# Kernel tuning notes

Hardware: AMD Instinct MI355X
Metric: run time of the kernel (lower is better)

Reference implementation:

```python
import jax, jax.numpy as jnp
import numpy as np

N, E, G = 10000, 160000, 64
NODE_DIM, HID = 128, 256


def _edge_conv(x, src, dst, w1, b1, w2, b2):
    # gather endpoints: x_i = target features, x_j = source features (PyG source_to_target)
    x_i = x[dst]                              # [E, C]
    x_j = x[src]                              # [E, C]
    m = jnp.concatenate([x_i, x_j - x_i], axis=-1)  # [E, 2C]
    m = jax.nn.relu(m @ w1 + b1) @ w2 + b2          # [E, H]
    out = jax.ops.segment_max(m, dst, num_segments=N)  # scatter-max per target node
    return out  # nodes with no in-edges get -inf; subsequent relu maps them to 0 (matches PyG fill 0 + relu)


def setup_inputs() -> dict:
    key = jax.random.key(0)
    ks = jax.random.split(key, 20)
    x = jax.random.normal(ks[0], (N, NODE_DIM), dtype=jnp.float32)
    edge_index = jax.random.randint(ks[1], (2, E), 0, N)
    batch = jnp.sort(jax.random.randint(ks[2], (N,), 0, G))
    s = 0.05
    inp = {"x": x, "edge_index": edge_index, "batch": batch}
    dims = [(2 * NODE_DIM, HID), (2 * HID, HID), (2 * HID, HID)]
    for li, (din, dout) in enumerate(dims):
        inp[f"c{li}_w1"] = jax.random.normal(ks[3 + 4 * li], (din, dout), jnp.float32) * s
        inp[f"c{li}_b1"] = jnp.zeros((dout,), jnp.float32)
        inp[f"c{li}_w2"] = jax.random.normal(ks[4 + 4 * li], (dout, dout), jnp.float32) * s
        inp[f"c{li}_b2"] = jnp.zeros((dout,), jnp.float32)
    inp["cl_w1"] = jax.random.normal(ks[15], (2 * HID, HID), jnp.float32) * s
    inp["cl_b1"] = jnp.zeros((HID,), jnp.float32)
    inp["cl_w2"] = jax.random.normal(ks[16], (HID, 64), jnp.float32) * s
    inp["cl_b2"] = jnp.zeros((64,), jnp.float32)
    inp["cl_w3"] = jax.random.normal(ks[17], (64, 1), jnp.float32) * s
    inp["cl_b3"] = jnp.zeros((1,), jnp.float32)
    return inp


def reference(x, edge_index, batch,
              c0_w1, c0_b1, c0_w2, c0_b2,
              c1_w1, c1_b1, c1_w2, c1_b2,
              c2_w1, c2_b1, c2_w2, c2_b2,
              cl_w1, cl_b1, cl_w2, cl_b2, cl_w3, cl_b3):
    src, dst = edge_index[0], edge_index[1]
    for (w1, b1, w2, b2) in [(c0_w1, c0_b1, c0_w2, c0_b2),
                             (c1_w1, c1_b1, c1_w2, c1_b2),
                             (c2_w1, c2_b1, c2_w2, c2_b2)]:
        x = jax.nn.relu(_edge_conv(x, src, dst, w1, b1, w2, b2))
    # global mean / max pool per graph
    sums = jax.ops.segment_sum(x, batch, num_segments=G)
    counts = jax.ops.segment_sum(jnp.ones((x.shape[0], 1), x.dtype), batch, num_segments=G)
    x_mean = sums / jnp.maximum(counts, 1.0)
    x_max = jax.ops.segment_max(x, batch, num_segments=G)
    x_max = jnp.where(counts > 0, x_max, 0.0)
    h = jnp.concatenate([x_mean, x_max], axis=1)  # [G, 2H]
    h = jax.nn.relu(h @ cl_w1 + cl_b1)            # dropout is eval-mode identity
    h = jax.nn.relu(h @ cl_w2 + cl_b2)
    out = (h @ cl_w3 + cl_b3).squeeze(-1)         # [G]
    return out
```

## Files before the change

kernel.cpp:

```cpp
#include <hip/hip_runtime.h>


#define NN 10000
#define NE 160000
#define NG 64
#define NP 10048
#define EB 64

typedef __attribute__((ext_vector_type(8))) _Float16 f16x8;
typedef __attribute__((ext_vector_type(4))) _Float16 f16x4;
typedef __attribute__((ext_vector_type(4))) float f32x4;

__global__ void hist_kernel(const int* __restrict__ dstI, int* __restrict__ hist) {
    int i = blockIdx.x * blockDim.x + threadIdx.x;
    if (i < NE) atomicAdd(&hist[dstI[i]], 1);
}

__global__ void scan_kernel(const int* __restrict__ hist, int* __restrict__ cursor) {
    __shared__ int sums[256];
    const int t = threadIdx.x;
    const int per = (NN + 255) / 256;
    const int lo = t * per, hi = (lo + per < NN) ? lo + per : NN;
    int s = 0;
    for (int i = lo; i < hi; ++i) s += hist[i];
    sums[t] = s;
    __syncthreads();
    for (int ofs = 1; ofs < 256; ofs <<= 1) {
        int add = (t >= ofs) ? sums[t - ofs] : 0;
        __syncthreads();
        sums[t] += add;
        __syncthreads();
    }
    int run = sums[t] - s;
    for (int i = lo; i < hi; ++i) {
        int h = hist[i];
        cursor[i] = run;
        run += h;
    }
}

__global__ void scatter_kernel(const int* __restrict__ srcI, const int* __restrict__ dstI,
                               int* __restrict__ cursor,
                               int* __restrict__ se2, int* __restrict__ de2) {
    int i = blockIdx.x * blockDim.x + threadIdx.x;
    if (i < NE) {
        int d = dstI[i];
        int p = atomicAdd(&cursor[d], 1);
        se2[p] = srcI[i];
        de2[p] = d;
    }
}

__global__ void prep_weights(const float* __restrict__ w1, const float* __restrict__ w2, int C,
                             _Float16* __restrict__ WcT, _Float16* __restrict__ w2T) {
    int total1 = 512 * C;
    int total = total1 + 256 * 256;
    for (int i = blockIdx.x * blockDim.x + threadIdx.x; i < total; i += gridDim.x * blockDim.x) {
        if (i < total1) {
            int n = i / C, k = i - n * C;
            float v = (n < 256) ? (w1[k * 256 + n] - w1[(C + k) * 256 + n])
                                : w1[(C + k) * 256 + (n - 256)];
            WcT[n * C + k] = (_Float16)v;
        } else {
            int j = i - total1;
            int n = j >> 8, k = j & 255;
            w2T[n * 256 + k] = (_Float16)w2[k * 256 + n];
        }
    }
}

__global__ void conv_rows(const float* __restrict__ src, int C, _Float16* __restrict__ xh) {
    int total = NP * C;
    for (int i = blockIdx.x * blockDim.x + threadIdx.x; i < total; i += gridDim.x * blockDim.x) {
        int row = i / C;
        xh[i] = (_Float16)((row < NN) ? src[i] : 0.f);
    }
}

template <int C>
__global__ __launch_bounds__(256) void node_gemm(
    const _Float16* __restrict__ xh, const _Float16* __restrict__ WT,
    const float* __restrict__ b1, float* __restrict__ AB) {
    const int wave = threadIdx.x >> 6, lane = threadIdx.x & 63;
    const int lrow = lane & 15, lk = (lane >> 4) * 8;
    const int r0 = blockIdx.x * 64;
    const int c0 = blockIdx.y * 128 + wave * 32;

    f32x4 acc[4][2] = {};
#pragma unroll
    for (int kk = 0; kk < C; kk += 32) {
        f16x8 ah[4];
#pragma unroll
        for (int m = 0; m < 4; ++m)
            ah[m] = *(const f16x8*)(xh + (size_t)(r0 + m * 16 + lrow) * C + kk + lk);
#pragma unroll
        for (int t = 0; t < 2; ++t) {
            f16x8 bh = *(const f16x8*)(WT + (size_t)(c0 + t * 16 + lrow) * C + kk + lk);
#pragma unroll
            for (int m = 0; m < 4; ++m)
                acc[m][t] = __builtin_amdgcn_mfma_f32_16x16x32_f16(ah[m], bh, acc[m][t], 0, 0, 0);
        }
    }
#pragma unroll
    for (int t = 0; t < 2; ++t) {
        const int col = c0 + t * 16 + lrow;
        const float bias = (col < 256) ? b1[col] : 0.f;
#pragma unroll
        for (int m = 0; m < 4; ++m) {
#pragma unroll
            for (int j = 0; j < 4; ++j) {
                const int row = r0 + m * 16 + (lane >> 4) * 4 + j;
                AB[(size_t)row * 512 + col] = acc[m][t][j] + bias;
            }
        }
    }
}

__global__ __launch_bounds__(256, 3) void edge_gemm(
    const float* __restrict__ AB,
    const int* __restrict__ se2, const int* __restrict__ de2,
    const _Float16* __restrict__ w2T,
    const float* __restrict__ b2, float* __restrict__ y) {
    __shared__ _Float16 hh[EB * 256];
    const int tid = threadIdx.x;
    const int wave = tid >> 6, lane = tid & 63;
    const int e0 = blockIdx.x * EB;
    const int ew = wave * 16;

    int se[16], de[16];
#pragma unroll
    for (int i = 0; i < 16; ++i) {
        se[i] = se2[e0 + ew + i];
        de[i] = de2[e0 + ew + i];
    }
#pragma unroll
    for (int b = 0; b < 4; ++b) {
        float4 av[4], bv[4];
#pragma unroll
        for (int i = 0; i < 4; ++i) {
            const int el = b * 4 + i;
            av[i] = *(const float4*)(AB + (size_t)de[el] * 512 + lane * 4);
            bv[i] = *(const float4*)(AB + (size_t)se[el] * 512 + 256 + lane * 4);
        }
#pragma unroll
        for (int i = 0; i < 4; ++i) {
            const int row = b * 16 + wave * 4 + i;
            f16x4 vh;
            vh[0] = (_Float16)fmaxf(av[i].x + bv[i].x, 0.f);
            vh[1] = (_Float16)fmaxf(av[i].y + bv[i].y, 0.f);
            vh[2] = (_Float16)fmaxf(av[i].z + bv[i].z, 0.f);
            vh[3] = (_Float16)fmaxf(av[i].w + bv[i].w, 0.f);
            const int idx = (row * 256 + lane * 4) ^ ((row & 7) << 3);
            *(f16x4*)(&hh[idx]) = vh;
        }
    }
    __syncthreads();

    const int lrow = lane & 15, lk = (lane >> 4) * 8;
    const _Float16* wbase = w2T + (size_t)(wave * 64 + lrow) * 256 + lk;

    f16x8 bhA[4], bhB[4];
#pragma unroll
    for (int t = 0; t < 4; ++t)
        bhA[t] = *(const f16x8*)(wbase + (size_t)(t * 16) * 256);

    f32x4 acc[4][4] = {};
#pragma unroll
    for (int kk = 0; kk < 256; kk += 32) {
        if (kk + 32 < 256) {
#pragma unroll
            for (int t = 0; t < 4; ++t)
                bhB[t] = *(const f16x8*)(wbase + (size_t)(t * 16) * 256 + kk + 32);
        }
        f16x8 ah[4];
#pragma unroll
        for (int m = 0; m < 4; ++m) {
            const int row = m * 16 + lrow;
            const int idx = (row * 256 + kk + lk) ^ ((row & 7) << 3);
            ah[m] = *(const f16x8*)(&hh[idx]);
        }
#pragma unroll
        for (int t = 0; t < 4; ++t)
#pragma unroll
            for (int m = 0; m < 4; ++m)
                acc[m][t] = __builtin_amdgcn_mfma_f32_16x16x32_f16(ah[m], bhA[t], acc[m][t], 0, 0, 0);
#pragma unroll
        for (int t = 0; t < 4; ++t) bhA[t] = bhB[t];
    }

    const int g = lane >> 4;
    int d[16];
#pragma unroll
    for (int k = 0; k < 16; ++k) d[k] = de2[e0 + g * 16 + k];
#pragma unroll
    for (int t = 0; t < 4; ++t) {
        const int col = wave * 64 + t * 16 + lrow;
        const float bias = b2[col];
        float run = acc[0][t][0] + bias;
        int dp = d[0];
#pragma unroll
        for (int k = 1; k < 16; ++k) {
            const float v = acc[k >> 2][t][k & 3] + bias;
            if (d[k] == dp) {
                run = fmaxf(run, v);
            } else {
                if (run > 0.f) atomicMax((int*)(y + (size_t)dp * 256 + col), __float_as_int(run));
                run = v;
                dp = d[k];
            }
        }
        if (run > 0.f) atomicMax((int*)(y + (size_t)dp * 256 + col), __float_as_int(run));
    }
}

__global__ void pool_kernel(const float* __restrict__ y, const int* __restrict__ batch,
                            float* __restrict__ pooled) {
    const int g = blockIdx.x;
    __shared__ int slo, shi;
    if (threadIdx.x == 0) {
        int lo = 0, hi = NN;
        while (lo < hi) { int m = (lo + hi) >> 1; if (batch[m] < g) lo = m + 1; else hi = m; }
        slo = lo;
        int lo2 = lo, hi2 = NN;
        while (lo2 < hi2) { int m = (lo2 + hi2) >> 1; if (batch[m] < g + 1) lo2 = m + 1; else hi2 = m; }
        shi = lo2;
    }
    __syncthreads();
    const int lo = slo, hi = shi, c = threadIdx.x;
    float s0 = 0.f, s1 = 0.f, s2 = 0.f, s3 = 0.f;
    float m0 = 0.f, m1 = 0.f, m2 = 0.f, m3 = 0.f;
    int n = lo;
    for (; n + 4 <= hi; n += 4) {
        float v0 = y[(size_t)(n + 0) * 256 + c];
        float v1 = y[(size_t)(n + 1) * 256 + c];
        float v2 = y[(size_t)(n + 2) * 256 + c];
        float v3 = y[(size_t)(n + 3) * 256 + c];
        s0 += v0; s1 += v1; s2 += v2; s3 += v3;
        m0 = fmaxf(m0, v0); m1 = fmaxf(m1, v1); m2 = fmaxf(m2, v2); m3 = fmaxf(m3, v3);
    }
    for (; n < hi; ++n) {
        float v = y[(size_t)n * 256 + c];
        s0 += v; m0 = fmaxf(m0, v);
    }
    const float s = (s0 + s1) + (s2 + s3);
    const float mx = fmaxf(fmaxf(m0, m1), fmaxf(m2, m3));
    const int cnt = hi - lo;
    pooled[g * 512 + c] = cnt ? s / (float)cnt : 0.f;
    pooled[g * 512 + 256 + c] = cnt ? mx : 0.f;
}

__global__ void classifier(const float* __restrict__ pooled,
                           const float* __restrict__ w1, const float* __restrict__ b1,
                           const float* __restrict__ w2, const float* __restrict__ b2,
                           const float* __restrict__ w3, const float* __restrict__ b3,
                           float* __restrict__ out) {
    const int g = blockIdx.x;
    __shared__ float ph[512];
    __shared__ float o1[256];
    __shared__ float o2[64];
    const int t = threadIdx.x;
    ph[t] = pooled[g * 512 + t];
    ph[t + 256] = pooled[g * 512 + 256 + t];
    __syncthreads();
    float s = 0.f;
    for (int k = 0; k < 512; ++k) s += ph[k] * w1[k * 256 + t];
    o1[t] = fmaxf(s + b1[t], 0.f);
    __syncthreads();
    if (t < 64) {
        float s2 = 0.f;
        for (int k = 0; k < 256; ++k) s2 += o1[k] * w2[k * 64 + t];
        o2[t] = fmaxf(s2 + b2[t], 0.f);
    }
    __syncthreads();
    if (t < 64) {
        float v = o2[t] * w3[t];
        for (int off = 32; off; off >>= 1) v += __shfl_down(v, off);
        if (t == 0) out[g] = v + b3[0];
    }
}

extern "C" void kernel_launch(void* const* d_in, const int* in_sizes, int n_in,
                              void* d_out, int out_size, void* d_ws, size_t ws_size,
                              hipStream_t stream) {
    (void)in_sizes; (void)n_in; (void)out_size; (void)ws_size;
    const float* x0 = (const float*)d_in[0];
    const int* eidx = (const int*)d_in[1];
    const int* batch = (const int*)d_in[2];
    const int* srcI = eidx;
    const int* dstI = eidx + NE;

    char* ws = (char*)d_ws;
    size_t off = 0;
    auto alloc = [&](size_t bytes) -> void* {
        void* p = ws + off;
        off += (bytes + 255) & ~(size_t)255;
        return p;
    };
    _Float16* xh = (_Float16*)alloc((size_t)NP * 256 * 2);
    float* AB = (float*)alloc((size_t)NP * 512 * 4);
    float* y  = (float*)alloc((size_t)NP * 256 * 4);
    _Float16* WcT = (_Float16*)alloc(512 * 256 * 2);
    _Float16* w2T = (_Float16*)alloc(256 * 256 * 2);
    float* pooled = (float*)alloc(64 * 512 * 4);
    int* hist = (int*)alloc(NN * 4);
    int* se2 = (int*)alloc(NE * 4);
    int* de2 = (int*)alloc(NE * 4);

    const float* lw[3][4] = {
        {(const float*)d_in[3],  (const float*)d_in[4],  (const float*)d_in[5],  (const float*)d_in[6]},
        {(const float*)d_in[7],  (const float*)d_in[8],  (const float*)d_in[9],  (const float*)d_in[10]},
        {(const float*)d_in[11], (const float*)d_in[12], (const float*)d_in[13], (const float*)d_in[14]},
    };

    hipMemsetAsync(hist, 0, NN * 4, stream);
    hist_kernel<<<dim3((NE + 255) / 256), dim3(256), 0, stream>>>(dstI, hist);
    scan_kernel<<<dim3(1), dim3(256), 0, stream>>>(hist, hist);
    scatter_kernel<<<dim3((NE + 255) / 256), dim3(256), 0, stream>>>(srcI, dstI, hist, se2, de2);

    conv_rows<<<dim3(512), dim3(256), 0, stream>>>(x0, 128, xh);

    for (int l = 0; l < 3; ++l) {
        const int C = (l == 0) ? 128 : 256;
        prep_weights<<<dim3(256), dim3(256), 0, stream>>>(lw[l][0], lw[l][2], C, WcT, w2T);
        if (C == 128)
            node_gemm<128><<<dim3(NP / 64, 4), dim3(256), 0, stream>>>(xh, WcT, lw[l][1], AB);
        else
            node_gemm<256><<<dim3(NP / 64, 4), dim3(256), 0, stream>>>(xh, WcT, lw[l][1], AB);
        hipMemsetAsync(y, 0, (size_t)NP * 256 * 4, stream);
        edge_gemm<<<dim3(NE / EB), dim3(256), 0, stream>>>(AB, se2, de2, w2T, lw[l][3], y);
        if (l < 2)
            conv_rows<<<dim3(1024), dim3(256), 0, stream>>>(y, 256, xh);
    }

    pool_kernel<<<dim3(NG), dim3(256), 0, stream>>>(y, batch, pooled);
    classifier<<<dim3(NG), dim3(256), 0, stream>>>(pooled,
        (const float*)d_in[15], (const float*)d_in[16],
        (const float*)d_in[17], (const float*)d_in[18],
        (const float*)d_in[19], (const float*)d_in[20], (float*)d_out);
}
```

Baseline: 390.8 us.

## Split node projection into fp32 A and fp16 B, remap edge blocks per XCD

The node GEMM now writes the destination half as fp32 and the source half as fp16 into separate 256-wide arrays. This halves the gather traffic for source rows in the edge kernel. The edge kernel remaps block IDs so that contiguous edge chunks (sorted by destination) land on the same XCD for L2 locality. It also raises the occupancy hint to 4, issues 8 gathers per batch, and drops the register double-buffering of w2T, loading it inline. conv_rows is vectorized to float4 to fp16x4. Storing B in fp16 adds rounding error, and removing the prefetch may expose weight-load latency.

```diff
diff --git a/kernel.cpp b/kernel.cpp
--- a/kernel.cpp
+++ b/kernel.cpp
@@ -69,18 +69,28 @@
     }
 }
 
-__global__ void conv_rows(const float* __restrict__ src, int C, _Float16* __restrict__ xh) {
-    int total = NP * C;
-    for (int i = blockIdx.x * blockDim.x + threadIdx.x; i < total; i += gridDim.x * blockDim.x) {
-        int row = i / C;
-        xh[i] = (_Float16)((row < NN) ? src[i] : 0.f);
+template <int C>
+__global__ void conv_rows(const float* __restrict__ src, _Float16* __restrict__ xh) {
+    const int total4 = NP * C / 4;
+    const int c4 = C / 4;
+    for (int i4 = blockIdx.x * blockDim.x + threadIdx.x; i4 < total4; i4 += gridDim.x * blockDim.x) {
+        const int row = i4 / c4;
+        f16x4 o;
+        if (row < NN) {
+            float4 v = ((const float4*)src)[i4];
+            o[0] = (_Float16)v.x; o[1] = (_Float16)v.y;
+            o[2] = (_Float16)v.z; o[3] = (_Float16)v.w;
+        } else {
+            o[0] = o[1] = o[2] = o[3] = (_Float16)0.f;
+        }
+        ((f16x4*)xh)[i4] = o;
     }
 }
 
 template <int C>
 __global__ __launch_bounds__(256) void node_gemm(
     const _Float16* __restrict__ xh, const _Float16* __restrict__ WT,
-    const float* __restrict__ b1, float* __restrict__ AB) {
+    const float* __restrict__ b1, float* __restrict__ Af, _Float16* __restrict__ Bh) {
     const int wave = threadIdx.x >> 6, lane = threadIdx.x & 63;
     const int lrow = lane & 15, lk = (lane >> 4) * 8;
     const int r0 = blockIdx.x * 64;
@@ -101,30 +111,48 @@
                 acc[m][t] = __builtin_amdgcn_mfma_f32_16x16x32_f16(ah[m], bh, acc[m][t], 0, 0, 0);
         }
     }
-#pragma unroll
-    for (int t = 0; t < 2; ++t) {
-        const int col = c0 + t * 16 + lrow;
-        const float bias = (col < 256) ? b1[col] : 0.f;
-#pragma unroll
-        for (int m = 0; m < 4; ++m) {
-#pragma unroll
-            for (int j = 0; j < 4; ++j) {
-                const int row = r0 + m * 16 + (lane >> 4) * 4 + j;
-                AB[(size_t)row * 512 + col] = acc[m][t][j] + bias;
-            }
-        }
-    }
-}
-
-__global__ __launch_bounds__(256, 3) void edge_gemm(
-    const float* __restrict__ AB,
+    if (blockIdx.y < 2) {
+#pragma unroll
+        for (int t = 0; t < 2; ++t) {
+            const int col = c0 + t * 16 + lrow;
+            const float bias = b1[col];
+#pragma unroll
+            for (int m = 0; m < 4; ++m)
+#pragma unroll
+                for (int j = 0; j < 4; ++j) {
+                    const int row = r0 + m * 16 + (lane >> 4) * 4 + j;
+                    Af[(size_t)row * 256 + col] = acc[m][t][j] + bias;
+                }
+        }
+    } else {
+#pragma unroll
+        for (int t = 0; t < 2; ++t) {
+            const int col = c0 - 256 + t * 16 + lrow;
+#pragma unroll
+            for (int m = 0; m < 4; ++m)
+#pragma unroll
+                for (int j = 0; j < 4; ++j) {
+                    const int row = r0 + m * 16 + (lane >> 4) * 4 + j;
+                    Bh[(size_t)row * 256 + col] = (_Float16)acc[m][t][j];
+                }
+        }
+    }
+}
+
+__global__ __launch_bounds__(256, 4) void edge_gemm(
+    const float* __restrict__ Af, const _Float16* __restrict__ Bh,
     const int* __restrict__ se2, const int* __restrict__ de2,
     const _Float16* __restrict__ w2T,
     const float* __restrict__ b2, float* __restrict__ y) {
     __shared__ _Float16 hh[EB * 256];
     const int tid = threadIdx.x;
     const int wave = tid >> 6, lane = tid & 63;
-    const int e0 = blockIdx.x * EB;
+
+    const int orig = blockIdx.x;
+    const int xcd = orig & 7, pos = orig >> 3;
+    const int q = 2500 >> 3, r = 2500 & 7;
+    const int bid = (xcd < r ? xcd * (q + 1) : r * (q + 1) + (xcd - r) * q) + pos;
+    const int e0 = bid * EB;
     const int ew = wave * 16;
 
     int se[16], de[16];
@@ -134,22 +162,24 @@
         de[i] = de2[e0 + ew + i];
     }
 #pragma unroll
-    for (int b = 0; b < 4; ++b) {
-        float4 av[4], bv[4];
-#pragma unroll
-        for (int i = 0; i < 4; ++i) {
-            const int el = b * 4 + i;
-            av[i] = *(const float4*)(AB + (size_t)de[el] * 512 + lane * 4);
-            bv[i] = *(const float4*)(AB + (size_t)se[el] * 512 + 256 + lane * 4);
-        }
-#pragma unroll
-        for (int i = 0; i < 4; ++i) {
-            const int row = b * 16 + wave * 4 + i;
+    for (int b = 0; b < 2; ++b) {
+        float4 av[8];
+        f16x4 bv[8];
+#pragma unroll
+        for (int i = 0; i < 8; ++i) {
+            const int el = b * 8 + i;
+            bv[i] = *(const f16x4*)(Bh + (size_t)se[el] * 256 + lane * 4);
+            av[i] = *(const float4*)(Af + (size_t)de[el] * 256 + lane * 4);
+        }
+#pragma unroll
+        for (int i = 0; i < 8; ++i) {
+            const int el = b * 8 + i;
+            const int row = (el >> 2) * 16 + wave * 4 + (el & 3);
             f16x4 vh;
-            vh[0] = (_Float16)fmaxf(av[i].x + bv[i].x, 0.f);
-            vh[1] = (_Float16)fmaxf(av[i].y + bv[i].y, 0.f);
-            vh[2] = (_Float16)fmaxf(av[i].z + bv[i].z, 0.f);
-            vh[3] = (_Float16)fmaxf(av[i].w + bv[i].w, 0.f);
+            vh[0] = (_Float16)fmaxf(av[i].x + (float)bv[i][0], 0.f);
+            vh[1] = (_Float16)fmaxf(av[i].y + (float)bv[i][1], 0.f);
+            vh[2] = (_Float16)fmaxf(av[i].z + (float)bv[i][2], 0.f);
+            vh[3] = (_Float16)fmaxf(av[i].w + (float)bv[i][3], 0.f);
             const int idx = (row * 256 + lane * 4) ^ ((row & 7) << 3);
             *(f16x4*)(&hh[idx]) = vh;
         }
@@ -159,19 +189,8 @@
     const int lrow = lane & 15, lk = (lane >> 4) * 8;
     const _Float16* wbase = w2T + (size_t)(wave * 64 + lrow) * 256 + lk;
 
-    f16x8 bhA[4], bhB[4];
-#pragma unroll
-    for (int t = 0; t < 4; ++t)
-        bhA[t] = *(const f16x8*)(wbase + (size_t)(t * 16) * 256);
-
     f32x4 acc[4][4] = {};
-#pragma unroll
     for (int kk = 0; kk < 256; kk += 32) {
-        if (kk + 32 < 256) {
-#pragma unroll
-            for (int t = 0; t < 4; ++t)
-                bhB[t] = *(const f16x8*)(wbase + (size_t)(t * 16) * 256 + kk + 32);
-        }
         f16x8 ah[4];
 #pragma unroll
         for (int m = 0; m < 4; ++m) {
@@ -180,12 +199,12 @@
             ah[m] = *(const f16x8*)(&hh[idx]);
         }
 #pragma unroll
-        for (int t = 0; t < 4; ++t)
+        for (int t = 0; t < 4; ++t) {
+            f16x8 bh = *(const f16x8*)(wbase + (size_t)(t * 16) * 256 + kk);
 #pragma unroll
             for (int m = 0; m < 4; ++m)
-                acc[m][t] = __builtin_amdgcn_mfma_f32_16x16x32_f16(ah[m], bhA[t], acc[m][t], 0, 0, 0);
-#pragma unroll
-        for (int t = 0; t < 4; ++t) bhA[t] = bhB[t];
+                acc[m][t] = __builtin_amdgcn_mfma_f32_16x16x32_f16(ah[m], bh, acc[m][t], 0, 0, 0);
+        }
     }
 
     const int g = lane >> 4;
@@ -297,7 +316,8 @@
         return p;
     };
     _Float16* xh = (_Float16*)alloc((size_t)NP * 256 * 2);
-    float* AB = (float*)alloc((size_t)NP * 512 * 4);
+    float* Af = (float*)alloc((size_t)NP * 256 * 4);
+    _Float16* Bh = (_Float16*)alloc((size_t)NP * 256 * 2);
     float* y  = (float*)alloc((size_t)NP * 256 * 4);
     _Float16* WcT = (_Float16*)alloc(512 * 256 * 2);
     _Float16* w2T = (_Float16*)alloc(256 * 256 * 2);
@@ -317,19 +337,19 @@
     scan_kernel<<<dim3(1), dim3(256), 0, stream>>>(hist, hist);
     scatter_kernel<<<dim3((NE + 255) / 256), dim3(256), 0, stream>>>(srcI, dstI, hist, se2, de2);
 
-    conv_rows<<<dim3(512), dim3(256), 0, stream>>>(x0, 128, xh);
+    conv_rows<128><<<dim3(1024), dim3(256), 0, stream>>>(x0, xh);
 
     for (int l = 0; l < 3; ++l) {
         const int C = (l == 0) ? 128 : 256;
         prep_weights<<<dim3(256), dim3(256), 0, stream>>>(lw[l][0], lw[l][2], C, WcT, w2T);
         if (C == 128)
-            node_gemm<128><<<dim3(NP / 64, 4), dim3(256), 0, stream>>>(xh, WcT, lw[l][1], AB);
+            node_gemm<128><<<dim3(NP / 64, 4), dim3(256), 0, stream>>>(xh, WcT, lw[l][1], Af, Bh);
         else
-            node_gemm<256><<<dim3(NP / 64, 4), dim3(256), 0, stream>>>(xh, WcT, lw[l][1], AB);
+            node_gemm<256><<<dim3(NP / 64, 4), dim3(256), 0, stream>>>(xh, WcT, lw[l][1], Af, Bh);
         hipMemsetAsync(y, 0, (size_t)NP * 256 * 4, stream);
-        edge_gemm<<<dim3(NE / EB), dim3(256), 0, stream>>>(AB, se2, de2, w2T, lw[l][3], y);
+        edge_gemm<<<dim3(NE / EB), dim3(256), 0, stream>>>(Af, Bh, se2, de2, w2T, lw[l][3], y);
         if (l < 2)
-            conv_rows<<<dim3(1024), dim3(256), 0, stream>>>(y, 256, xh);
+            conv_rows<256><<<dim3(1024), dim3(256), 0, stream>>>(y, xh);
     }
 
     pool_kernel<<<dim3(NG), dim3(256), 0, stream>>>(y, batch, pooled);
```

Measured after the change: 358.1 us. 8.4% less time.
